# Kernel tuning notes

Measured on AMD Instinct MI355X. Metric: run time of the kernel, lower is better.

## Reference

```python
import jax, jax.numpy as jnp
import numpy as np

USER_NUM = 100000
ITEM_NUM = 100000
N = USER_NUM + ITEM_NUM
D = 64
N_EDGES = 3200000
N_LAYERS = 3
LAYER_CL = 1
EPS = 0.2


def setup_inputs() -> dict:
    key = jax.random.key(0)
    k1, k2, k3, k4, k5, k6 = jax.random.split(key, 6)
    user_emb = jax.random.normal(k1, (USER_NUM, D), dtype=jnp.float32)
    item_emb = jax.random.normal(k2, (ITEM_NUM, D), dtype=jnp.float32)
    adj_src = jax.random.randint(k3, (N_EDGES,), 0, N, dtype=jnp.int64)
    adj_dst = jax.random.randint(k4, (N_EDGES,), 0, N, dtype=jnp.int64)
    adj_vals = jax.random.uniform(k5, (N_EDGES,), dtype=jnp.float32)
    noise = jax.random.uniform(k6, (N_LAYERS, N, D), dtype=jnp.float32)
    return {"user_emb": user_emb, "item_emb": item_emb, "adj_src": adj_src,
            "adj_dst": adj_dst, "adj_vals": adj_vals, "noise": noise}


def reference(user_emb, item_emb, adj_src, adj_dst, adj_vals, noise):
    # ego_embeddings = cat([user_emb, item_emb])  -> [N, D]
    ego = jnp.concatenate([user_emb, item_emb], axis=0)
    acc = jnp.zeros_like(ego)
    cl = ego
    for k in range(N_LAYERS):
        # sparse.mm: out[dst] += val * ego[src]
        msg = ego[adj_src] * adj_vals[:, None]          # [E, D]
        ego = jax.ops.segment_sum(msg, adj_dst, num_segments=N)
        # perturbed noise injection: ego += sign(ego) * F.normalize(noise, dim=-1) * eps
        rn = noise[k]
        rn = rn / jnp.maximum(jnp.linalg.norm(rn, axis=-1, keepdims=True), 1e-12)
        ego = ego + jnp.sign(ego) * rn * EPS
        acc = acc + ego
        if k == LAYER_CL - 1:
            cl = ego
    final = acc / N_LAYERS  # mean over stacked layer outputs
    return (final[:USER_NUM], final[USER_NUM:], cl[:USER_NUM], cl[USER_NUM:])
```

## Files before the change

kernel.cpp:

```cpp
#include <hip/hip_runtime.h>

#define USER_NUM 100000
#define ITEM_NUM 100000
#define NN 200000
#define DIM 64
#define EPSV 0.2f

#define NB 196
#define BSH 10
#define NPB 1024
#define CH 4096
#define PER 16
#define SRC_MASK 0x3FFFF

__global__ __launch_bounds__(256) void bhist_k(const int* __restrict__ dst,
                                               int* __restrict__ bhist, int E) {
    __shared__ int h[NB];
    int t = threadIdx.x;
    for (int i = t; i < NB; i += 256) h[i] = 0;
    __syncthreads();
    long long base = (long long)blockIdx.x * CH;
    #pragma unroll
    for (int j = 0; j < PER; ++j) {
        long long e = base + t + j * 256;
        if (e < E) atomicAdd(&h[dst[e] >> BSH], 1);
    }
    __syncthreads();
    for (int i = t; i < NB; i += 256) if (h[i]) atomicAdd(&bhist[i], h[i]);
}

__global__ __launch_bounds__(256) void bscan_k(const int* __restrict__ bhist,
                                               int* __restrict__ bucket_base,
                                               int* __restrict__ bucket_off,
                                               int* __restrict__ row_ptr, int E) {
    __shared__ int tmp[256];
    int t = threadIdx.x;
    int s = (t < NB) ? bhist[t] : 0;
    tmp[t] = s;
    __syncthreads();
    for (int off = 1; off < 256; off <<= 1) {
        int x = (t >= off) ? tmp[t - off] : 0;
        __syncthreads();
        tmp[t] += x;
        __syncthreads();
    }
    int excl = tmp[t] - s;
    if (t < NB) { bucket_base[t] = excl; bucket_off[t] = excl; }
    if (t == 0) { bucket_base[NB] = E; row_ptr[NN] = E; }
}

__global__ __launch_bounds__(256) void apart_k(const int* __restrict__ src,
                                               const int* __restrict__ dst,
                                               const float* __restrict__ vals,
                                               int* __restrict__ bucket_off,
                                               int2* __restrict__ out, int E) {
    __shared__ int cnt[NB], start[NB], cursor[NB], gbase[NB];
    __shared__ int tmp[256];
    __shared__ int2 rec[CH];
    int t = threadIdx.x;
    long long base = (long long)blockIdx.x * CH;
    int nvalid = (int)min((long long)CH, (long long)E - base);

    int s_[PER]; int d_[PER]; float v_[PER];
    for (int i = t; i < NB; i += 256) cnt[i] = 0;
    __syncthreads();
    #pragma unroll
    for (int j = 0; j < PER; ++j) {
        int idx = t + j * 256;
        if (idx < nvalid) {
            long long e = base + idx;
            d_[j] = dst[e]; s_[j] = src[e]; v_[j] = vals[e];
            atomicAdd(&cnt[d_[j] >> BSH], 1);
        } else d_[j] = -1;
    }
    __syncthreads();
    int c = (t < NB) ? cnt[t] : 0;
    tmp[t] = c;
    __syncthreads();
    for (int off = 1; off < 256; off <<= 1) {
        int x = (t >= off) ? tmp[t - off] : 0;
        __syncthreads();
        tmp[t] += x;
        __syncthreads();
    }
    if (t < NB) {
        int excl = tmp[t] - c;
        start[t] = excl; cursor[t] = excl;
        gbase[t] = (c > 0) ? atomicAdd(&bucket_off[t], c) : 0;
    }
    __syncthreads();
    #pragma unroll
    for (int j = 0; j < PER; ++j) {
        if (d_[j] >= 0) {
            int b = d_[j] >> BSH;
            int slot = atomicAdd(&cursor[b], 1);
            rec[slot] = make_int2(s_[j] | ((d_[j] & (NPB - 1)) << 18),
                                  __float_as_int(v_[j]));
        }
    }
    __syncthreads();
    for (int slot = t; slot < nvalid; slot += 256) {
        int lo = 0, hi = NB - 1;
        while (lo < hi) {
            int mid = (lo + hi + 1) >> 1;
            if (start[mid] <= slot) lo = mid; else hi = mid - 1;
        }
        out[gbase[lo] + (slot - start[lo])] = rec[slot];
    }
}

__global__ __launch_bounds__(256) void bsort_k(const int* __restrict__ bucket_base,
                                               const int2* __restrict__ in,
                                               int2* __restrict__ out,
                                               int* __restrict__ row_ptr) {
    __shared__ int noff[NPB];
    __shared__ int tmp[256];
    int b = blockIdx.x, t = threadIdx.x;
    int rbeg = bucket_base[b], rend = bucket_base[b + 1];
    for (int i = t; i < NPB; i += 256) noff[i] = 0;
    __syncthreads();
    for (int i = rbeg + t; i < rend; i += 256)
        atomicAdd(&noff[(in[i].x >> 18) & (NPB - 1)], 1);
    __syncthreads();
    int l0 = noff[t * 4], l1 = noff[t * 4 + 1], l2 = noff[t * 4 + 2], l3 = noff[t * 4 + 3];
    int s = l0 + l1 + l2 + l3;
    tmp[t] = s;
    __syncthreads();
    for (int off = 1; off < 256; off <<= 1) {
        int x = (t >= off) ? tmp[t - off] : 0;
        __syncthreads();
        tmp[t] += x;
        __syncthreads();
    }
    int run = rbeg + tmp[t] - s;
    int e0 = run, e1 = run + l0, e2 = e1 + l1, e3 = e2 + l2;
    noff[t * 4] = e0; noff[t * 4 + 1] = e1; noff[t * 4 + 2] = e2; noff[t * 4 + 3] = e3;
    int node0 = b * NPB + t * 4;
    if (node0 < NN)     row_ptr[node0]     = e0;
    if (node0 + 1 < NN) row_ptr[node0 + 1] = e1;
    if (node0 + 2 < NN) row_ptr[node0 + 2] = e2;
    if (node0 + 3 < NN) row_ptr[node0 + 3] = e3;
    __syncthreads();
    for (int i = rbeg + t; i < rend; i += 256) {
        int2 r = in[i];
        int pos = atomicAdd(&noff[(r.x >> 18) & (NPB - 1)], 1);
        out[pos] = r;
    }
}

__global__ __launch_bounds__(256) void spmm_fused_k(const int* __restrict__ row_ptr,
                                                    const int2* __restrict__ ssv,
                                                    const float* __restrict__ ego_u,
                                                    const float* __restrict__ ego_i,
                                                    float* __restrict__ ego_out,
                                                    const float* __restrict__ nz_layer,
                                                    float* __restrict__ acc,
                                                    int is_first, int is_last) {
    int node = blockIdx.x * 4 + (threadIdx.x >> 6);
    int lane = threadIdx.x & 63;
    int g    = lane >> 4;
    int d4   = lane & 15;
    int beg = row_ptr[node];
    int end = row_ptr[node + 1];

    double ax = 0.0, ay = 0.0, az = 0.0, aw = 0.0;
    int base = beg;
    #pragma unroll 2
    for (; base + 4 <= end; base += 4) {
        int2 sv = ssv[base + g];
        int s = sv.x & SRC_MASK;
        double v = (double)__int_as_float(sv.y);
        const float* eb = (s < USER_NUM) ? ego_u : ego_i;
        const float4 r = *reinterpret_cast<const float4*>(eb + ((size_t)s << 6) + (d4 << 2));
        ax = fma((double)r.x, v, ax); ay = fma((double)r.y, v, ay);
        az = fma((double)r.z, v, az); aw = fma((double)r.w, v, aw);
    }
    int rem = end - base;
    if (g < rem) {
        int2 sv = ssv[base + g];
        int s = sv.x & SRC_MASK;
        double v = (double)__int_as_float(sv.y);
        const float* eb = (s < USER_NUM) ? ego_u : ego_i;
        const float4 r = *reinterpret_cast<const float4*>(eb + ((size_t)s << 6) + (d4 << 2));
        ax = fma((double)r.x, v, ax); ay = fma((double)r.y, v, ay);
        az = fma((double)r.z, v, az); aw = fma((double)r.w, v, aw);
    }
    ax += __shfl_xor(ax, 16, 64); ay += __shfl_xor(ay, 16, 64);
    az += __shfl_xor(az, 16, 64); aw += __shfl_xor(aw, 16, 64);
    ax += __shfl_xor(ax, 32, 64); ay += __shfl_xor(ay, 32, 64);
    az += __shfl_xor(az, 32, 64); aw += __shfl_xor(aw, 32, 64);
    float fx = (float)ax, fy = (float)ay, fz = (float)az, fw = (float)aw;

    size_t off = (size_t)node * DIM + (d4 << 2);
    const float4 nz = *reinterpret_cast<const float4*>(nz_layer + off);
    float ss = nz.x * nz.x + nz.y * nz.y + nz.z * nz.z + nz.w * nz.w;
    ss += __shfl_xor(ss, 1, 64);
    ss += __shfl_xor(ss, 2, 64);
    ss += __shfl_xor(ss, 4, 64);
    ss += __shfl_xor(ss, 8, 64);
    float e = EPSV / fmaxf(sqrtf(ss), 1e-12f);

    float4 val;
    val.x = fx + ((fx > 0.f) ? 1.f : ((fx < 0.f) ? -1.f : 0.f)) * nz.x * e;
    val.y = fy + ((fy > 0.f) ? 1.f : ((fy < 0.f) ? -1.f : 0.f)) * nz.y * e;
    val.z = fz + ((fz > 0.f) ? 1.f : ((fz < 0.f) ? -1.f : 0.f)) * nz.z * e;
    val.w = fw + ((fw > 0.f) ? 1.f : ((fw < 0.f) ? -1.f : 0.f)) * nz.w * e;

    if (g == 0) {
        if (!is_last) *reinterpret_cast<float4*>(ego_out + off) = val;
        float4 r4;
        if (is_first) {
            r4 = val;
        } else {
            const float4 p = *reinterpret_cast<const float4*>(acc + off);
            r4.x = p.x + val.x; r4.y = p.y + val.y;
            r4.z = p.z + val.z; r4.w = p.w + val.w;
        }
        if (is_last) {
            r4.x *= (1.0f / 3.0f); r4.y *= (1.0f / 3.0f);
            r4.z *= (1.0f / 3.0f); r4.w *= (1.0f / 3.0f);
        }
        *reinterpret_cast<float4*>(acc + off) = r4;
    }
}

extern "C" void kernel_launch(void* const* d_in, const int* in_sizes, int n_in,
                              void* d_out, int out_size, void* d_ws, size_t ws_size,
                              hipStream_t stream) {
    const float* user_emb = (const float*)d_in[0];
    const float* item_emb = (const float*)d_in[1];
    const int*   adj_src  = (const int*)d_in[2];
    const int*   adj_dst  = (const int*)d_in[3];
    const float* adj_vals = (const float*)d_in[4];
    const float* noise    = (const float*)d_in[5];
    const int E = in_sizes[2];

    const long long ND = (long long)NN * DIM;
    float* out_final = (float*)d_out;
    float* out_cl    = out_final + ND;

    char*  w       = (char*)d_ws;
    float* ego_a   = (float*)w;
    int2*  ssv_b   = (int2*)w;
    int2*  ssv     = (int2*)(w + ND * sizeof(float));
    int*   bhist   = (int*)(ssv + E);
    int*   bbase   = bhist + NB;
    int*   boff    = bbase + NB + 1;
    int*   row_ptr = boff + NB;

    const int nchunk = (E + CH - 1) / CH;

    hipMemsetAsync(bhist, 0, NB * sizeof(int), stream);
    bhist_k<<<nchunk, 256, 0, stream>>>(adj_dst, bhist, E);
    bscan_k<<<1, 256, 0, stream>>>(bhist, bbase, boff, row_ptr, E);
    apart_k<<<nchunk, 256, 0, stream>>>(adj_src, adj_dst, adj_vals, boff, ssv_b, E);
    bsort_k<<<NB, 256, 0, stream>>>(bbase, ssv_b, ssv, row_ptr);

    const int spmm_grid = NN / 4;
    const float* item_shift = item_emb - (long long)USER_NUM * DIM;
    spmm_fused_k<<<spmm_grid, 256, 0, stream>>>(row_ptr, ssv, user_emb, item_shift,
                                                out_cl, noise, out_final, 1, 0);
    spmm_fused_k<<<spmm_grid, 256, 0, stream>>>(row_ptr, ssv, out_cl, out_cl,
                                                ego_a, noise + ND, out_final, 0, 0);
    spmm_fused_k<<<spmm_grid, 256, 0, stream>>>(row_ptr, ssv, ego_a, ego_a,
                                                nullptr, noise + 2 * ND, out_final, 0, 1);
}
```

Before: 793.6 us.

## Gather embeddings as bf16 in SpMM layers and unroll edge loop by four

Adds a conversion kernel that packs the initial embeddings into bf16, and has each SpMM layer write its output embedding in bf16 to ping-pong buffers. The gathers read half the bytes per edge. Accumulation stays in double, and the cl output is still written in fp32 from the first layer. The edge loop is also unrolled to issue four independent gathers per lane group. This halves random-gather traffic but adds bf16 rounding error to the propagated embeddings, which may exceed tolerance, and adds an extra conversion pass.

```diff
diff --git a/kernel.cpp b/kernel.cpp
--- a/kernel.cpp
+++ b/kernel.cpp
@@ -148,11 +148,31 @@
     }
 }
 
+__device__ __forceinline__ unsigned int bpack(float a, float b) {
+    unsigned int ua = __float_as_uint(a), ub = __float_as_uint(b);
+    ua = (ua + 0x7fffu + ((ua >> 16) & 1u)) >> 16;
+    ub = (ub + 0x7fffu + ((ub >> 16) & 1u)) >> 16;
+    return ua | (ub << 16);
+}
+
+__global__ __launch_bounds__(256) void cvt_k(const float* __restrict__ ue,
+                                             const float* __restrict__ ie,
+                                             unsigned int* __restrict__ out) {
+    long long i = (long long)blockIdx.x * 256 + threadIdx.x;
+    const long long tot = (long long)NN * (DIM / 4);
+    if (i >= tot) return;
+    const long long uu = (long long)USER_NUM * (DIM / 4);
+    const float4 v = (i < uu) ? reinterpret_cast<const float4*>(ue)[i]
+                              : reinterpret_cast<const float4*>(ie)[i - uu];
+    uint2 p; p.x = bpack(v.x, v.y); p.y = bpack(v.z, v.w);
+    reinterpret_cast<uint2*>(out)[i] = p;
+}
+
 __global__ __launch_bounds__(256) void spmm_fused_k(const int* __restrict__ row_ptr,
                                                     const int2* __restrict__ ssv,
-                                                    const float* __restrict__ ego_u,
-                                                    const float* __restrict__ ego_i,
-                                                    float* __restrict__ ego_out,
+                                                    const unsigned int* __restrict__ ego,
+                                                    unsigned int* __restrict__ ego_out,
+                                                    float* __restrict__ cl_out,
                                                     const float* __restrict__ nz_layer,
                                                     float* __restrict__ acc,
                                                     int is_first, int is_last) {
@@ -165,25 +185,60 @@
 
     double ax = 0.0, ay = 0.0, az = 0.0, aw = 0.0;
     int base = beg;
-    #pragma unroll 2
+
+    for (; base + 16 <= end; base += 16) {
+        int2 sv0 = ssv[base + g];
+        int2 sv1 = ssv[base + 4 + g];
+        int2 sv2 = ssv[base + 8 + g];
+        int2 sv3 = ssv[base + 12 + g];
+        int s0 = sv0.x & SRC_MASK, s1 = sv1.x & SRC_MASK;
+        int s2 = sv2.x & SRC_MASK, s3 = sv3.x & SRC_MASK;
+        const uint2 q0 = *reinterpret_cast<const uint2*>(ego + ((size_t)s0 << 5) + (d4 << 1));
+        const uint2 q1 = *reinterpret_cast<const uint2*>(ego + ((size_t)s1 << 5) + (d4 << 1));
+        const uint2 q2 = *reinterpret_cast<const uint2*>(ego + ((size_t)s2 << 5) + (d4 << 1));
+        const uint2 q3 = *reinterpret_cast<const uint2*>(ego + ((size_t)s3 << 5) + (d4 << 1));
+        double v0 = (double)__int_as_float(sv0.y);
+        double v1 = (double)__int_as_float(sv1.y);
+        double v2 = (double)__int_as_float(sv2.y);
+        double v3 = (double)__int_as_float(sv3.y);
+        float f0, f1, f2, f3;
+        f0 = __uint_as_float(q0.x << 16); f1 = __uint_as_float(q0.x & 0xffff0000u);
+        f2 = __uint_as_float(q0.y << 16); f3 = __uint_as_float(q0.y & 0xffff0000u);
+        ax = fma((double)f0, v0, ax); ay = fma((double)f1, v0, ay);
+        az = fma((double)f2, v0, az); aw = fma((double)f3, v0, aw);
+        f0 = __uint_as_float(q1.x << 16); f1 = __uint_as_float(q1.x & 0xffff0000u);
+        f2 = __uint_as_float(q1.y << 16); f3 = __uint_as_float(q1.y & 0xffff0000u);
+        ax = fma((double)f0, v1, ax); ay = fma((double)f1, v1, ay);
+        az = fma((double)f2, v1, az); aw = fma((double)f3, v1, aw);
+        f0 = __uint_as_float(q2.x << 16); f1 = __uint_as_float(q2.x & 0xffff0000u);
+        f2 = __uint_as_float(q2.y << 16); f3 = __uint_as_float(q2.y & 0xffff0000u);
+        ax = fma((double)f0, v2, ax); ay = fma((double)f1, v2, ay);
+        az = fma((double)f2, v2, az); aw = fma((double)f3, v2, aw);
+        f0 = __uint_as_float(q3.x << 16); f1 = __uint_as_float(q3.x & 0xffff0000u);
+        f2 = __uint_as_float(q3.y << 16); f3 = __uint_as_float(q3.y & 0xffff0000u);
+        ax = fma((double)f0, v3, ax); ay = fma((double)f1, v3, ay);
+        az = fma((double)f2, v3, az); aw = fma((double)f3, v3, aw);
+    }
     for (; base + 4 <= end; base += 4) {
         int2 sv = ssv[base + g];
         int s = sv.x & SRC_MASK;
         double v = (double)__int_as_float(sv.y);
-        const float* eb = (s < USER_NUM) ? ego_u : ego_i;
-        const float4 r = *reinterpret_cast<const float4*>(eb + ((size_t)s << 6) + (d4 << 2));
-        ax = fma((double)r.x, v, ax); ay = fma((double)r.y, v, ay);
-        az = fma((double)r.z, v, az); aw = fma((double)r.w, v, aw);
+        const uint2 q = *reinterpret_cast<const uint2*>(ego + ((size_t)s << 5) + (d4 << 1));
+        float f0 = __uint_as_float(q.x << 16), f1 = __uint_as_float(q.x & 0xffff0000u);
+        float f2 = __uint_as_float(q.y << 16), f3 = __uint_as_float(q.y & 0xffff0000u);
+        ax = fma((double)f0, v, ax); ay = fma((double)f1, v, ay);
+        az = fma((double)f2, v, az); aw = fma((double)f3, v, aw);
     }
     int rem = end - base;
     if (g < rem) {
         int2 sv = ssv[base + g];
         int s = sv.x & SRC_MASK;
         double v = (double)__int_as_float(sv.y);
-        const float* eb = (s < USER_NUM) ? ego_u : ego_i;
-        const float4 r = *reinterpret_cast<const float4*>(eb + ((size_t)s << 6) + (d4 << 2));
-        ax = fma((double)r.x, v, ax); ay = fma((double)r.y, v, ay);
-        az = fma((double)r.z, v, az); aw = fma((double)r.w, v, aw);
+        const uint2 q = *reinterpret_cast<const uint2*>(ego + ((size_t)s << 5) + (d4 << 1));
+        float f0 = __uint_as_float(q.x << 16), f1 = __uint_as_float(q.x & 0xffff0000u);
+        float f2 = __uint_as_float(q.y << 16), f3 = __uint_as_float(q.y & 0xffff0000u);
+        ax = fma((double)f0, v, ax); ay = fma((double)f1, v, ay);
+        az = fma((double)f2, v, az); aw = fma((double)f3, v, aw);
     }
     ax += __shfl_xor(ax, 16, 64); ay += __shfl_xor(ay, 16, 64);
     az += __shfl_xor(az, 16, 64); aw += __shfl_xor(aw, 16, 64);
@@ -207,7 +262,11 @@
     val.w = fw + ((fw > 0.f) ? 1.f : ((fw < 0.f) ? -1.f : 0.f)) * nz.w * e;
 
     if (g == 0) {
-        if (!is_last) *reinterpret_cast<float4*>(ego_out + off) = val;
+        if (!is_last) {
+            uint2 p; p.x = bpack(val.x, val.y); p.y = bpack(val.z, val.w);
+            *reinterpret_cast<uint2*>(ego_out + ((size_t)node << 5) + (d4 << 1)) = p;
+        }
+        if (cl_out) *reinterpret_cast<float4*>(cl_out + off) = val;
         float4 r4;
         if (is_first) {
             r4 = val;
@@ -239,11 +298,13 @@
     float* out_final = (float*)d_out;
     float* out_cl    = out_final + ND;
 
-    char*  w       = (char*)d_ws;
-    float* ego_a   = (float*)w;
-    int2*  ssv_b   = (int2*)w;
-    int2*  ssv     = (int2*)(w + ND * sizeof(float));
-    int*   bhist   = (int*)(ssv + E);
+    char* w = (char*)d_ws;
+    const long long B16 = (long long)NN * (DIM / 2) * 4;
+    unsigned int* egoB0 = (unsigned int*)w;
+    int2*         ssv_b = (int2*)w;
+    unsigned int* egoB1 = (unsigned int*)(w + B16);
+    int2*         ssv   = (int2*)(w + 2 * B16);
+    int*   bhist   = (int*)(w + 3 * B16);
     int*   bbase   = bhist + NB;
     int*   boff    = bbase + NB + 1;
     int*   row_ptr = boff + NB;
@@ -255,13 +316,14 @@
     bscan_k<<<1, 256, 0, stream>>>(bhist, bbase, boff, row_ptr, E);
     apart_k<<<nchunk, 256, 0, stream>>>(adj_src, adj_dst, adj_vals, boff, ssv_b, E);
     bsort_k<<<NB, 256, 0, stream>>>(bbase, ssv_b, ssv, row_ptr);
+    cvt_k<<<(int)(((long long)NN * (DIM / 4) + 255) / 256), 256, 0, stream>>>(
+        user_emb, item_emb, egoB0);
 
     const int spmm_grid = NN / 4;
-    const float* item_shift = item_emb - (long long)USER_NUM * DIM;
-    spmm_fused_k<<<spmm_grid, 256, 0, stream>>>(row_ptr, ssv, user_emb, item_shift,
+    spmm_fused_k<<<spmm_grid, 256, 0, stream>>>(row_ptr, ssv, egoB0, egoB1,
                                                 out_cl, noise, out_final, 1, 0);
-    spmm_fused_k<<<spmm_grid, 256, 0, stream>>>(row_ptr, ssv, out_cl, out_cl,
-                                                ego_a, noise + ND, out_final, 0, 0);
-    spmm_fused_k<<<spmm_grid, 256, 0, stream>>>(row_ptr, ssv, ego_a, ego_a,
+    spmm_fused_k<<<spmm_grid, 256, 0, stream>>>(row_ptr, ssv, egoB1, egoB0,
+                                                nullptr, noise + ND, out_final, 0, 0);
+    spmm_fused_k<<<spmm_grid, 256, 0, stream>>>(row_ptr, ssv, egoB0, nullptr,
                                                 nullptr, noise + 2 * ND, out_final, 0, 1);
 }
```

Measured after the change: 778.7 us. No clear change (-1.9%).
